# Optimization experiments

Hardware: AMD Instinct MI355X
Metric: run time of the kernel (lower is better)

The kernel has to match this reference:

```python
import math
import jax, jax.numpy as jnp
import numpy as np
from jax import lax

B, IMG, CIN, ED, TD, M = 32, 224, 3, 64, 64, 32
DILATIONS = (1, 2, 3, 4)
KS, STRIDE = 7, 4


def _conv2d(x, w, b, stride, pad, dil=1):
    y = lax.conv_general_dilated(x, w, (stride, stride), [(pad, pad), (pad, pad)],
                                 rhs_dilation=(dil, dil),
                                 dimension_numbers=('NCHW', 'OIHW', 'NCHW'))
    return y + b[None, :, None, None]


def _ln(x, g, b):
    mu = x.mean(-1, keepdims=True)
    var = ((x - mu) ** 2).mean(-1, keepdims=True)
    return (x - mu) / jnp.sqrt(var + 1e-5) * g + b


def setup_inputs() -> dict:
    key = jax.random.key(0)
    ks = jax.random.split(key, 25)
    s = 0.05
    rn = lambda k, shp: (jax.random.normal(k, shp) * s).astype(jnp.float32)
    inp = {}
    inp['x'] = jax.random.normal(ks[0], (B, CIN, IMG, IMG), dtype=jnp.float32)
    # PRM dilated conv weights (stacked over 4 dilations)
    inp['prm_w'] = rn(ks[1], (4, ED, CIN, KS, KS))
    inp['prm_b'] = rn(ks[2], (4, ED))
    # PCM stem: conv-SiLU, conv-BN-SiLU, conv-SiLU
    inp['pcm_w1'] = rn(ks[3], (ED, CIN, 3, 3))
    inp['pcm_b1'] = rn(ks[4], (ED,))
    inp['pcm_w2'] = rn(ks[5], (ED, ED, 3, 3))
    inp['pcm_b2'] = rn(ks[6], (ED,))
    inp['bn_g'] = 1.0 + rn(ks[7], (ED,))
    inp['bn_b'] = rn(ks[8], (ED,))
    inp['bn_mean'] = rn(ks[9], (ED,))
    inp['bn_var'] = jax.random.uniform(ks[10], (ED,), minval=0.5, maxval=1.5).astype(jnp.float32)
    inp['pcm_w3'] = rn(ks[11], (TD, ED, 3, 3))
    inp['pcm_b3'] = rn(ks[12], (TD,))
    # Token_performer params (dim = 4*ED = 256, emb = TD = 64, m = 32)
    dim = 4 * ED
    inp['ln1_g'] = 1.0 + rn(ks[13], (dim,))
    inp['ln1_b'] = rn(ks[14], (dim,))
    inp['kqv_w'] = rn(ks[15], (3 * TD, dim))
    inp['kqv_b'] = rn(ks[16], (3 * TD,))
    # orthogonal random-feature matrix, rows orthonormal, scaled by sqrt(m)
    a = np.random.default_rng(0).normal(size=(TD, TD))
    qmat, _ = np.linalg.qr(a)
    inp['w_perf'] = jnp.asarray(qmat[:M] * math.sqrt(M), dtype=jnp.float32)
    inp['proj_w'] = rn(ks[17], (TD, TD))
    inp['proj_b'] = rn(ks[18], (TD,))
    inp['ln2_g'] = 1.0 + rn(ks[19], (TD,))
    inp['ln2_b'] = rn(ks[20], (TD,))
    inp['mlp_w1'] = rn(ks[21], (TD, TD))
    inp['mlp_b1'] = rn(ks[22], (TD,))
    inp['mlp_w2'] = rn(ks[23], (TD, TD))
    inp['mlp_b2'] = rn(ks[24], (TD,))
    inp['H'] = IMG
    inp['W'] = IMG
    return inp


def reference(x, prm_w, prm_b, pcm_w1, pcm_b1, pcm_w2, pcm_b2, bn_g, bn_b, bn_mean,
              bn_var, pcm_w3, pcm_b3, ln1_g, ln1_b, kqv_w, kqv_b, w_perf, proj_w,
              proj_b, ln2_g, ln2_b, mlp_w1, mlp_b1, mlp_w2, mlp_b2, H, W):
    Bx = x.shape[0]
    Hp, Wp = H // STRIDE, W // STRIDE
    # --- PRM: parallel dilated Conv2d + GELU branches ---
    branches = []
    for i, d in enumerate(DILATIONS):  # fixed small set of structurally distinct convs
        pad = math.ceil(((KS - 1) * d + 1 - STRIDE) / 2)
        branches.append(jax.nn.gelu(_conv2d(x, prm_w[i], prm_b[i], STRIDE, pad, d),
                                    approximate=False))
    y = jnp.stack(branches, axis=1)  # [B, 4, ED, Hp, Wp]
    prm_x = y.reshape(Bx, len(DILATIONS) * ED, Hp * Wp).transpose(0, 2, 1)  # [B, N, 256]
    # --- PCM stem: conv-SiLU / conv-BN-SiLU / conv-SiLU (eval-mode BN) ---
    c = jax.nn.silu(_conv2d(x, pcm_w1, pcm_b1, 2, 1))
    c = _conv2d(c, pcm_w2, pcm_b2, 2, 1)
    inv = (bn_g / jnp.sqrt(bn_var + 1e-5))[None, :, None, None]
    c = (c - bn_mean[None, :, None, None]) * inv + bn_b[None, :, None, None]
    c = jax.nn.silu(c)
    c = jax.nn.silu(_conv2d(c, pcm_w3, pcm_b3, 1, 1))  # [B, TD, Hp, Wp]
    convX = c.transpose(0, 2, 3, 1).reshape(Bx, Hp * Wp, TD)
    # --- Performer kernelized attention ---
    xn = _ln(prm_x, ln1_g, ln1_b)
    kqv = xn @ kqv_w.T + kqv_b
    k, q, v = kqv[..., :TD], kqv[..., TD:2 * TD], kqv[..., 2 * TD:]

    def prm_exp(z):
        xd = 0.5 * (z * z).sum(-1, keepdims=True)          # [B, N, 1]
        wtx = jnp.einsum('bti,mi->btm', z, w_perf)          # [B, N, M]
        return jnp.exp(wtx - xd) / math.sqrt(M)

    kp, qp = prm_exp(k), prm_exp(q)                         # [B, N, M]
    D = jnp.einsum('btm,bm->bt', qp, kp.sum(axis=1))[..., None]  # [B, N, 1]
    kptv = jnp.einsum('btn,btm->bnm', v, kp)                # [B, TD, M]
    ya = jnp.einsum('btm,bnm->btn', qp, kptv) / (D + 1e-8)  # [B, N, TD]
    ya = v + ya @ proj_w.T + proj_b
    # --- combine + MLP block ---
    xo = ya + convX
    h = _ln(xo, ln2_g, ln2_b)
    h = jax.nn.gelu(h @ mlp_w1.T + mlp_b1, approximate=False) @ mlp_w2.T + mlp_b2
    return xo + h
```

## Files before the change

### kernel.cpp

```cpp
#include <hip/hip_runtime.h>
#include <hip/hip_bf16.h>
#include <cstddef>

#define BB    32
#define IMG   224
#define CIN   3
#define ED    64
#define TD    64
#define MM    32
#define HP    56
#define TT    3136
#define C4    256
#define KQVN  192

typedef __attribute__((ext_vector_type(8))) short bf16x8;
typedef __attribute__((ext_vector_type(4))) float f32x4;

#define OFF_CONVX  0u
#define OFF_XN     6422528u
#define OFF_C2B    6422528u
#define OFF_C1B    19267584u
#define OFF_V      19267584u
#define OFF_KP     25690112u
#define OFF_QP     28901376u
#define OFF_PART   32112640u
#define OFF_KPTV   33161216u
#define OFF_KPSP   (OFF_KPTV + 32768u)
#define OFF_WPJB   (OFF_KPTV + 49152u)
#define OFF_WM1B   (OFF_KPTV + 51200u)
#define OFF_WM2B   (OFF_KPTV + 53248u)
#define OFF_KPSUM  33226752u
#define OFF_WPT    (OFF_PART)
#define OFF_WKB    (OFF_PART + 37632u)
#define OFF_WC2B   (OFF_PART + 62208u)
#define OFF_WT3B   (OFF_PART + 80640u)
#define OFF_WC1B   (OFF_PART + 99072u)

__device__ __forceinline__ float geluf(float v){
  return 0.5f*v*(1.f + erff(v*0.70710678118654752f));
}
__device__ __forceinline__ float siluf(float v){
  return v/(1.f + expf(-v));
}
__device__ __forceinline__ ushort bfbits(float v){
  __hip_bfloat16 h = __float2bfloat16(v);
  return *reinterpret_cast<ushort*>(&h);
}

__global__ __launch_bounds__(256) void k_wtrans(
    const float* __restrict__ prm_w, const float* __restrict__ kqv_w,
    const float* __restrict__ pcm_w2, const float* __restrict__ pcm_w3,
    const float* __restrict__ pcm_w1, const float* __restrict__ proj_w,
    const float* __restrict__ mlp_w1, const float* __restrict__ mlp_w2,
    float* __restrict__ wpt, __hip_bfloat16* __restrict__ wkb,
    __hip_bfloat16* __restrict__ wc2b, __hip_bfloat16* __restrict__ wt3b,
    __hip_bfloat16* __restrict__ wc1b, __hip_bfloat16* __restrict__ wpjb,
    __hip_bfloat16* __restrict__ wm1b, __hip_bfloat16* __restrict__ wm2b)
{
  int idx = blockIdx.x*256 + threadIdx.x;
  if (idx < 37632){
    int oc = idx & 63, r = idx >> 6;
    int i = r/147, tap = r - i*147;
    wpt[idx] = prm_w[(i*64 + oc)*147 + tap];
  } else if (idx < 86784){
    int i4 = idx - 37632;
    wkb[i4] = __float2bfloat16(kqv_w[i4]);
  } else if (idx < 123648){
    int i2 = idx - 86784;
    int oc = i2/576, rem = i2 - oc*576;
    int khkw = rem >> 6, ci = rem & 63;
    int kh = khkw/3, kw = khkw - kh*3;
    wc2b[i2] = __float2bfloat16(pcm_w2[(oc*64+ci)*9 + kh*3 + kw]);
  } else if (idx < 160512){
    int i3 = idx - 123648;
    int oc = i3/576, rem = i3 - oc*576;
    int khkw = rem >> 6, ci = rem & 63;
    int kh = khkw/3, kw = khkw - kh*3;
    wt3b[i3] = __float2bfloat16(pcm_w3[(oc*64+ci)*9 + kh*3 + kw]);
  } else if (idx < 162560){
    int i5 = idx - 160512;
    int oc = i5 >> 5, k = i5 & 31;
    float v = 0.f;
    if (k < 27) v = pcm_w1[oc*27 + k];
    wc1b[i5] = __float2bfloat16(v);
  } else if (idx < 166656){
    wpjb[idx - 162560] = __float2bfloat16(proj_w[idx - 162560]);
  } else if (idx < 170752){
    wm1b[idx - 166656] = __float2bfloat16(mlp_w1[idx - 166656]);
  } else if (idx < 174848){
    wm2b[idx - 170752] = __float2bfloat16(mlp_w2[idx - 170752]);
  }
}

__global__ __launch_bounds__(256) void k_conv1(
    const float* __restrict__ x, const __hip_bfloat16* __restrict__ wc1b,
    const float* __restrict__ bias, __hip_bfloat16* __restrict__ c1b)
{
  __shared__ __align__(16) ushort xs[3*17*18];
  __shared__ __align__(16) ushort As[64*40];
  const int t = threadIdx.x;
  const int b = blockIdx.y;
  const int th = blockIdx.x/14, tw = blockIdx.x - th*14;
  const int oh0 = th*8, ow0 = tw*8;
  const int ih0 = oh0*2 - 1, iw0 = ow0*2 - 1;
  const int w = t>>6, lane = t&63, l15 = lane&15, hi = lane>>4;

  const float* xb = x + (size_t)b*CIN*IMG*IMG;
  for (int idx = t; idx < 918; idx += 256){
    int ci = idx/306, rem = idx - ci*306;
    int r = rem/18, c = rem - r*18;
    float v = 0.f;
    int ih = ih0 + r, iw = iw0 + c;
    if (c < 17 && (unsigned)ih < 224u && (unsigned)iw < 224u)
      v = xb[(ci*IMG+ih)*IMG+iw];
    xs[idx] = bfbits(v);
  }
  __syncthreads();
  for (int idx = t; idx < 2048; idx += 256){
    int pos = idx >> 5, k = idx & 31;
    ushort v = 0;
    if (k < 27){
      int ci = k/9, rem = k - ci*9;
      int kh = rem/3, kw = rem - kh*3;
      v = xs[(ci*17 + (pos>>3)*2 + kh)*18 + (pos&7)*2 + kw];
    }
    As[pos*40 + k] = v;
  }
  __syncthreads();

  float bs4[4];
  #pragma unroll
  for (int nb=0;nb<4;++nb) bs4[nb] = bias[nb*16+l15];
  f32x4 acc[4];
  #pragma unroll
  for (int nb=0;nb<4;++nb) acc[nb] = (f32x4){0.f,0.f,0.f,0.f};
  const ushort* wq = (const ushort*)wc1b;
  {
    bf16x8 a = *(const bf16x8*)&As[(w*16+l15)*40 + hi*8];
    #pragma unroll
    for (int nb=0;nb<4;++nb){
      bf16x8 bv = *(const bf16x8*)&wq[(nb*16+l15)*32 + hi*8];
      acc[nb] = __builtin_amdgcn_mfma_f32_16x16x32_bf16(a, bv, acc[nb], 0, 0, 0);
    }
  }
  #pragma unroll
  for (int nb=0;nb<4;++nb){
    #pragma unroll
    for (int r=0;r<4;++r){
      int row = w*16 + hi*4 + r;
      int oh = oh0 + (row>>3), ow = ow0 + (row&7);
      c1b[(((size_t)b*112+oh)*112+ow)*64 + nb*16+l15] =
        __float2bfloat16(siluf(acc[nb][r] + bs4[nb]));
    }
  }
}

__global__ __launch_bounds__(256) void k_conv2(
    const __hip_bfloat16* __restrict__ c1b, const __hip_bfloat16* __restrict__ wc2b,
    const float* __restrict__ bias, const float* __restrict__ g,
    const float* __restrict__ bb, const float* __restrict__ mean,
    const float* __restrict__ var, __hip_bfloat16* __restrict__ c2b)
{
  __shared__ __align__(16) ushort xs[17*17*72];
  const int b = blockIdx.y;
  const int th = blockIdx.x/7, tw = blockIdx.x - th*7;
  const int oh0 = th*8, ow0 = tw*8;
  const int t = threadIdx.x;
  const int w = t>>6, lane = t&63, l15 = lane&15, hi = lane>>4;

  const int ih0 = oh0*2-1, iw0 = ow0*2-1;
  const ushort* c1u = (const ushort*)c1b;
  for (int seg = t; seg < 2312; seg += 256){
    int pos = seg >> 3, s8 = seg & 7;
    int r = pos/17, c = pos - r*17;
    int ih = ih0 + r, iw = iw0 + c;
    uint4 val = {0,0,0,0};
    if ((unsigned)ih < 112u && (unsigned)iw < 112u)
      val = *(const uint4*)&c1u[(((size_t)b*112+ih)*112+iw)*64 + s8*8];
    *(uint4*)&xs[(r*17+c)*72 + s8*8] = val;
  }
  __syncthreads();

  float bs4[4], iv4[4], mn4[4], bo4[4];
  #pragma unroll
  for (int nb=0;nb<4;++nb){
    int oc = nb*16+l15;
    bs4[nb] = bias[oc];
    iv4[nb] = g[oc]*rsqrtf(var[oc]+1e-5f);
    mn4[nb] = mean[oc];
    bo4[nb] = bb[oc];
  }

  f32x4 acc[4];
  #pragma unroll
  for (int nb=0;nb<4;++nb) acc[nb] = (f32x4){0.f,0.f,0.f,0.f};

  const int p = w*16 + l15, pr = p>>3, pc = p&7;
  const ushort* wq = (const ushort*)wc2b;

  for (int ks=0; ks<18; ++ks){
    const int k0 = ks*32 + hi*8;
    const int khkw = k0 >> 6, ci0 = k0 & 63;
    const int kh = khkw/3, kw = khkw - kh*3;
    bf16x8 a = *(const bf16x8*)&xs[((2*pr+kh)*17 + 2*pc+kw)*72 + ci0];
    #pragma unroll
    for (int nb=0;nb<4;++nb){
      bf16x8 bv = *(const bf16x8*)&wq[(nb*16+l15)*576 + k0];
      acc[nb] = __builtin_amdgcn_mfma_f32_16x16x32_bf16(a, bv, acc[nb], 0, 0, 0);
    }
  }

  #pragma unroll
  for (int nb=0;nb<4;++nb){
    #pragma unroll
    for (int r=0;r<4;++r){
      int pp = w*16 + hi*4 + r;
      int oh = oh0 + (pp>>3), ow = ow0 + (pp&7);
      float vv = acc[nb][r] + bs4[nb];
      vv = (vv - mn4[nb])*iv4[nb] + bo4[nb];
      c2b[(((size_t)b*56+oh)*56+ow)*64 + nb*16+l15] = __float2bfloat16(siluf(vv));
    }
  }
}

__global__ __launch_bounds__(256) void k_conv3(
    const __hip_bfloat16* __restrict__ c2b, const __hip_bfloat16* __restrict__ wt3b,
    const float* __restrict__ bias, float* __restrict__ convX)
{
  __shared__ __align__(16) ushort xs[10*12*72];
  const int b = blockIdx.y;
  const int th = blockIdx.x/7, tw = blockIdx.x - th*7;
  const int oh0 = th*8, ow0 = tw*8;
  const int t = threadIdx.x;
  const int w = t>>6, lane = t&63, l15 = lane&15, hi = lane>>4;

  const ushort* c2u = (const ushort*)c2b;
  for (int seg = t; seg < 960; seg += 256){
    int pos = seg >> 3, s8 = seg & 7;
    int r = pos/12, c = pos - r*12;
    int ih = oh0 - 1 + r, iw = ow0 - 1 + c;
    uint4 val = {0,0,0,0};
    if ((unsigned)ih < 56u && (unsigned)iw < 56u)
      val = *(const uint4*)&c2u[(((size_t)b*56+ih)*56+iw)*64 + s8*8];
    *(uint4*)&xs[(r*12+c)*72 + s8*8] = val;
  }
  __syncthreads();

  float bs4[4];
  #pragma unroll
  for (int nb=0;nb<4;++nb) bs4[nb] = bias[nb*16+l15];

  f32x4 acc[4];
  #pragma unroll
  for (int nb=0;nb<4;++nb) acc[nb] = (f32x4){0.f,0.f,0.f,0.f};

  const int p = w*16 + l15, pr = p>>3, pc = p&7;
  const ushort* wq = (const ushort*)wt3b;

  for (int ks=0; ks<18; ++ks){
    const int k0 = ks*32 + hi*8;
    const int khkw = k0 >> 6, ci0 = k0 & 63;
    const int kh = khkw/3, kw = khkw - kh*3;
    bf16x8 a = *(const bf16x8*)&xs[((pr+kh)*12 + pc+kw)*72 + ci0];
    #pragma unroll
    for (int nb=0;nb<4;++nb){
      bf16x8 bv = *(const bf16x8*)&wq[(nb*16+l15)*576 + k0];
      acc[nb] = __builtin_amdgcn_mfma_f32_16x16x32_bf16(a, bv, acc[nb], 0, 0, 0);
    }
  }

  #pragma unroll
  for (int nb=0;nb<4;++nb){
    #pragma unroll
    for (int r=0;r<4;++r){
      int pp = w*16 + hi*4 + r;
      int oh = oh0 + (pp>>3), ow = ow0 + (pp&7);
      int s = oh*HP + ow;
      convX[((size_t)b*TT + s)*64 + nb*16+l15] = siluf(acc[nb][r] + bs4[nb]);
    }
  }
}

#define LOADX(PH) do{ const float4* xr_ = (const float4*)(rowb + (PH)*20); \
  *(float4*)&X[0]=xr_[0]; *(float4*)&X[4]=xr_[1]; *(float4*)&X[8]=xr_[2]; \
  *(float4*)&X[12]=xr_[3]; *(float4*)&X[16]=xr_[4]; }while(0)
#define TAP(KW,Q0) do{ const float wv_ = wrow[(KW)*64]; \
  v[0]+=wv_*X[(Q0)+0];  v[1]+=wv_*X[(Q0)+1];  v[2]+=wv_*X[(Q0)+2];  v[3]+=wv_*X[(Q0)+3]; \
  v[4]+=wv_*X[(Q0)+4];  v[5]+=wv_*X[(Q0)+5];  v[6]+=wv_*X[(Q0)+6];  v[7]+=wv_*X[(Q0)+7]; \
  v[8]+=wv_*X[(Q0)+8];  v[9]+=wv_*X[(Q0)+9];  v[10]+=wv_*X[(Q0)+10]; v[11]+=wv_*X[(Q0)+11]; \
  v[12]+=wv_*X[(Q0)+12]; v[13]+=wv_*X[(Q0)+13]; }while(0)

template<int D>
__device__ __forceinline__ void prm_core(const float* __restrict__ xt2,
    const float* __restrict__ wq, float v[14])
{
  constexpr int R0 = 12 - 3*D;
  #pragma unroll 1
  for (int ci=0; ci<3; ++ci){
    #pragma unroll 1
    for (int kh=0; kh<7; ++kh){
      const float* rowb = xt2 + ci*2000 + (R0 + kh*D)*80;
      const float* wrow = wq + ((ci*7+kh)*7)*64;
      float X[20];
      if constexpr (D == 1){
        LOADX(0); TAP(3,3);
        LOADX(1); TAP(0,2); TAP(4,3);
        LOADX(2); TAP(1,2); TAP(5,3);
        LOADX(3); TAP(2,2); TAP(6,3);
      } else if constexpr (D == 2){
        LOADX(0); TAP(1,2); TAP(3,3); TAP(5,4);
        LOADX(2); TAP(0,1); TAP(2,2); TAP(4,3); TAP(6,4);
      } else if constexpr (D == 3){
        LOADX(0); TAP(3,3);
        LOADX(1); TAP(2,2); TAP(6,5);
        LOADX(2); TAP(1,1); TAP(5,4);
        LOADX(3); TAP(0,0); TAP(4,3);
      } else {
        LOADX(0); TAP(0,0); TAP(1,1); TAP(2,2); TAP(3,3); TAP(4,4); TAP(5,5); TAP(6,6);
      }
    }
  }
}

__global__ __launch_bounds__(256) void k_prm_ln(
    const float* __restrict__ x, const float* __restrict__ wpt,
    const float* __restrict__ prm_b, const float* __restrict__ ln_g,
    const float* __restrict__ ln_b, __hip_bfloat16* __restrict__ xn)
{
  __shared__ __align__(16) float xt2[6000];
  __shared__ float wred[4][14][2];
  const int t = threadIdx.x;
  const int b = blockIdx.y;
  const int oh  = blockIdx.x >> 2;
  const int owt = blockIdx.x & 3;
  const int ow0 = owt*14;
  const int ih0 = oh*4 - 11;
  const int iw0 = ow0*4 - 11;

  const float* xb = x + (size_t)b*CIN*IMG*IMG;
  for (int idx = t; idx < 6000; idx += 256){
    int ci  = idx / 2000;
    int rem = idx - ci*2000;
    int r   = rem / 80;
    int cc  = rem - r*80;
    int ih = ih0 + r, iw = iw0 + cc;
    float val = 0.f;
    if ((unsigned)ih < (unsigned)IMG && (unsigned)iw < (unsigned)IMG)
      val = xb[(ci*IMG+ih)*IMG+iw];
    xt2[(ci*25 + r)*80 + (cc&3)*20 + (cc>>2)] = val;
  }
  __syncthreads();

  const int i = t >> 6, lane = t & 63;
  float v[14];
  const float bi = prm_b[i*64+lane];
  #pragma unroll
  for (int p=0;p<14;++p) v[p] = bi;
  const float* wq = wpt + (i*147)*64 + lane;

  if      (i == 0) prm_core<1>(xt2, wq, v);
  else if (i == 1) prm_core<2>(xt2, wq, v);
  else if (i == 2) prm_core<3>(xt2, wq, v);
  else             prm_core<4>(xt2, wq, v);

  #pragma unroll
  for (int p=0;p<14;++p) v[p] = geluf(v[p]);
  #pragma unroll
  for (int p=0;p<14;++p){
    float s1 = v[p], s2 = v[p]*v[p];
    #pragma unroll
    for (int o=32;o;o>>=1){
      s1 += __shfl_xor(s1, o, 64);
      s2 += __shfl_xor(s2, o, 64);
    }
    if (lane == 0){ wred[i][p][0] = s1; wred[i][p][1] = s2; }
  }
  __syncthreads();
  const float lg = ln_g[t], lb = ln_b[t];
  const int s_base = oh*HP + ow0;
  #pragma unroll
  for (int p=0;p<14;++p){
    float S1 = wred[0][p][0]+wred[1][p][0]+wred[2][p][0]+wred[3][p][0];
    float S2 = wred[0][p][1]+wred[1][p][1]+wred[2][p][1]+wred[3][p][1];
    float mu = S1*(1.f/256.f);
    float rs = rsqrtf(S2*(1.f/256.f) - mu*mu + 1e-5f);
    float outv = (v[p]-mu)*rs*lg + lb;
    xn[((size_t)(b*TT + s_base + p))*256 + t] = __float2bfloat16(outv);
  }
}

__global__ __launch_bounds__(256) void k_kqv_perf(
    const __hip_bfloat16* __restrict__ xn, const __hip_bfloat16* __restrict__ wkb,
    const float* __restrict__ kqv_b, const float* __restrict__ wperf,
    float* __restrict__ v_g, float* __restrict__ kp, float* __restrict__ qp)
{
  __shared__ __align__(16) char smem[36864];
  __shared__ float wperf_s[32*68];
  __shared__ float kqvb_s[192];
  __shared__ float xd_s[128];
  ushort* As = (ushort*)smem;
  ushort* Bs = (ushort*)(smem + 9216);
  float*  zq = (float*)smem;

  const int t = threadIdx.x;
  const int m0 = blockIdx.x*64;
  const int w = t >> 6, lane = t & 63;
  const int l15 = lane & 15, hi = lane >> 4;

  for (int idx = t; idx < 2048; idx += 256)
    wperf_s[(idx>>6)*68 + (idx&63)] = wperf[idx];
  if (t < 192) kqvb_s[t] = kqv_b[t];

  f32x4 acc[12];
  #pragma unroll
  for (int nb=0;nb<12;++nb) acc[nb] = (f32x4){0.f,0.f,0.f,0.f};

  const ushort* xnu = (const ushort*)xn;
  const ushort* wku = (const ushort*)wkb;

  for (int kc=0; kc<4; ++kc){
    #pragma unroll
    for (int ss=0; ss<2; ++ss){
      int seg = ss*256 + t;
      int row = seg >> 3, c8 = seg & 7;
      *(uint4*)&As[row*72 + c8*8] =
        *(const uint4*)&xnu[((size_t)(m0+row))*256 + kc*64 + c8*8];
    }
    #pragma unroll
    for (int ss=0; ss<6; ++ss){
      int seg = ss*256 + t;
      int row = seg >> 3, c8 = seg & 7;
      *(uint4*)&Bs[row*72 + c8*8] =
        *(const uint4*)&wku[row*256 + kc*64 + c8*8];
    }
    __syncthreads();
    #pragma unroll
    for (int ks=0; ks<2; ++ks){
      bf16x8 a = *(const bf16x8*)&As[(16*w + l15)*72 + ks*32 + hi*8];
      #pragma unroll
      for (int nb=0;nb<12;++nb){
        bf16x8 bv = *(const bf16x8*)&Bs[(nb*16 + l15)*72 + ks*32 + hi*8];
        acc[nb] = __builtin_amdgcn_mfma_f32_16x16x32_bf16(a, bv, acc[nb], 0, 0, 0);
      }
    }
    __syncthreads();
  }

  #pragma unroll
  for (int nb=0;nb<12;++nb){
    int col = nb*16 + l15;
    float bias = kqvb_s[col];
    #pragma unroll
    for (int r=0;r<4;++r){
      int row = w*16 + hi*4 + r;
      float val = acc[nb][r] + bias;
      if (col < 128) zq[row*132 + col] = val;
      else v_g[((size_t)(m0+row))*64 + (col-128)] = val;
    }
  }
  __syncthreads();

  if (t < 128){
    int pos = t & 63, wh = t >> 6;
    const float4* zr4 = (const float4*)&zq[pos*132 + wh*64];
    float s = 0.f;
    #pragma unroll
    for (int c4=0;c4<16;++c4){
      float4 z4 = zr4[c4];
      s += z4.x*z4.x + z4.y*z4.y + z4.z*z4.z + z4.w*z4.w;
    }
    xd_s[t] = 0.5f*s;
  }
  __syncthreads();

  {
    const int qi = t >> 1, mbase = (t & 1)*16;
    const int pos = qi & 63, wh = qi >> 6;
    const float4* zr4 = (const float4*)&zq[pos*132 + wh*64];
    float wtx[16];
    #pragma unroll
    for (int j=0;j<16;++j) wtx[j] = 0.f;
    #pragma unroll 4
    for (int c4=0;c4<16;++c4){
      float4 z4 = zr4[c4];
      #pragma unroll
      for (int j=0;j<16;++j){
        const float4 w4 = *(const float4*)&wperf_s[(mbase+j)*68 + c4*4];
        wtx[j] += z4.x*w4.x + z4.y*w4.y + z4.z*w4.z + z4.w*w4.w;
      }
    }
    const float xd = xd_s[qi];
    float* dst = wh ? qp : kp;
    float* dp = dst + ((size_t)(m0+pos))*32 + mbase;
    #pragma unroll
    for (int j4=0;j4<4;++j4){
      float4 o;
      o.x = expf(wtx[j4*4+0] - xd) * 0.17677669529663687f;
      o.y = expf(wtx[j4*4+1] - xd) * 0.17677669529663687f;
      o.z = expf(wtx[j4*4+2] - xd) * 0.17677669529663687f;
      o.w = expf(wtx[j4*4+3] - xd) * 0.17677669529663687f;
      *(float4*)&dp[j4*4] = o;
    }
  }
}

__global__ __launch_bounds__(256) void k_kptv(
    const float* __restrict__ v_g, const float* __restrict__ kp,
    float* __restrict__ part, float* __restrict__ kpsum_part)
{
  __shared__ __align__(16) ushort vT[64*232];
  __shared__ __align__(16) ushort kpT[32*232];
  __shared__ float ksh[8][32];
  const int b = blockIdx.y, g = blockIdx.x;
  const int t = threadIdx.x;
  const int w = t>>6, lane = t&63, l15 = lane&15, hi = lane>>4;
  const int t0 = g*196;

  for (int idx = t; idx < 14336; idx += 256){
    int tt = idx >> 6, n = idx & 63;
    float vv = (tt < 196) ? v_g[((size_t)b*TT + t0 + tt)*64 + n] : 0.f;
    vT[n*232 + tt] = bfbits(vv);
  }
  for (int idx = t; idx < 7168; idx += 256){
    int tt = idx >> 5, m = idx & 31;
    float kv = (tt < 196) ? kp[((size_t)b*TT + t0 + tt)*32 + m] : 0.f;
    kpT[m*232 + tt] = bfbits(kv);
  }
  __syncthreads();

  f32x4 accp[2];
  accp[0] = (f32x4){0.f,0.f,0.f,0.f};
  accp[1] = (f32x4){0.f,0.f,0.f,0.f};
  for (int ks=0; ks<7; ++ks){
    bf16x8 a = *(const bf16x8*)&vT[(w*16+l15)*232 + ks*32 + hi*8];
    #pragma unroll
    for (int nt=0; nt<2; ++nt){
      bf16x8 bv = *(const bf16x8*)&kpT[(nt*16+l15)*232 + ks*32 + hi*8];
      accp[nt] = __builtin_amdgcn_mfma_f32_16x16x32_bf16(a, bv, accp[nt], 0, 0, 0);
    }
  }
  #pragma unroll
  for (int nt=0;nt<2;++nt){
    #pragma unroll
    for (int r=0;r<4;++r){
      int row = w*16 + hi*4 + r;
      int col = nt*16 + l15;
      part[(((size_t)g*BB + b)*64 + row)*MM + col] = accp[nt][r];
    }
  }
  {
    int m = t & 31, h8 = t >> 5;
    float s = 0.f;
    int lo = h8*25, hic = lo+25 < 196 ? lo+25 : 196;
    for (int tt = lo; tt < hic; ++tt){
      ushort u = kpT[m*232 + tt];
      __hip_bfloat16 hv = *reinterpret_cast<__hip_bfloat16*>(&u);
      s += __bfloat162float(hv);
    }
    ksh[h8][m] = s;
  }
  __syncthreads();
  if (t < 32){
    float s = 0.f;
    #pragma unroll
    for (int j=0;j<8;++j) s += ksh[j][t];
    kpsum_part[(size_t)g*1024 + b*32 + t] = s;
  }
}

__global__ __launch_bounds__(256) void k_kptv_red(
    const float* __restrict__ part, const float* __restrict__ kpsum_part,
    __hip_bfloat16* __restrict__ kptvb, float* __restrict__ kpsum)
{
  const int t = threadIdx.x;
  const int idx = blockIdx.x*256 + t;
  float a = 0.f;
  #pragma unroll
  for (int g=0; g<16; ++g) a += part[(size_t)g*65536 + idx];
  kptvb[idx] = __float2bfloat16(a);
  if (blockIdx.x < 4){
    int kidx = blockIdx.x*256 + t;
    float s = 0.f;
    #pragma unroll
    for (int g=0; g<16; ++g) s += kpsum_part[(size_t)g*1024 + kidx];
    kpsum[kidx] = s;
  }
}

__global__ __launch_bounds__(256) void k_attn_mlp(
    const float* __restrict__ v_g, const float* __restrict__ qp,
    const float* __restrict__ kpsum, const __hip_bfloat16* __restrict__ kptvb,
    const __hip_bfloat16* __restrict__ wpjb, const float* __restrict__ projb,
    const float* __restrict__ convX,
    const float* __restrict__ ln2_g, const float* __restrict__ ln2_b,
    const __hip_bfloat16* __restrict__ wm1b, const float* __restrict__ b1,
    const __hip_bfloat16* __restrict__ wm2b, const float* __restrict__ b2,
    float* __restrict__ out)
{
  __shared__ __align__(16) char smem[64512];
  ushort* qpb = (ushort*)smem;
  ushort* ktb = (ushort*)(smem + 5120);
  ushort* pjw = (ushort*)(smem + 10240);
  ushort* hb  = (ushort*)smem;
  ushort* t2  = (ushort*)(smem + 19456);
  ushort* w1b = (ushort*)(smem + 28672);
  ushort* w2b = (ushort*)(smem + 37888);
  float*  xosh= (float*)(smem + 47104);
  __shared__ float Ds[64];
  __shared__ float Dp[4][64];
  __shared__ float ks_s[32], pjb_s[64], b1_s[64], b2_s[64], g2_s[64], bb2_s[64];

  const int t = threadIdx.x;
  const int b = blockIdx.y;
  const int p0 = blockIdx.x*64;
  const int w = t>>6, lane = t&63, l15 = lane&15, hi = lane>>4;

  const float* qpg = qp + ((size_t)b*TT + p0)*32;
  for (int idx = t; idx < 2048; idx += 256)
    qpb[(idx>>5)*40 + (idx&31)] = bfbits(qpg[idx]);
  const ushort* ktg = (const ushort*)kptvb + (size_t)b*2048;
  for (int idx = t; idx < 2048; idx += 256)
    ktb[(idx>>5)*40 + (idx&31)] = ktg[idx];
  const ushort* pju = (const ushort*)wpjb;
  const ushort* w1u = (const ushort*)wm1b;
  const ushort* w2u = (const ushort*)wm2b;
  for (int idx = t; idx < 4096; idx += 256){
    pjw[(idx>>6)*72 + (idx&63)] = pju[idx];
    w1b[(idx>>6)*72 + (idx&63)] = w1u[idx];
    w2b[(idx>>6)*72 + (idx&63)] = w2u[idx];
  }
  if (t < 32) ks_s[t] = kpsum[b*MM + t];
  if (t < 64){
    pjb_s[t] = projb[t]; b1_s[t] = b1[t]; b2_s[t] = b2[t];
    g2_s[t] = ln2_g[t];  bb2_s[t] = ln2_b[t];
  }
  __syncthreads();

  {
    int pos = t & 63, grp = t >> 6;
    float s = 0.f;
    #pragma unroll
    for (int j=0;j<8;++j){
      int m = grp*8 + j;
      __hip_bfloat16 h = *reinterpret_cast<__hip_bfloat16*>(&qpb[pos*40 + m]);
      s += __bfloat162float(h) * ks_s[m];
    }
    Dp[grp][pos] = s;
  }
  __syncthreads();
  if (t < 64) Ds[t] = Dp[0][t]+Dp[1][t]+Dp[2][t]+Dp[3][t] + 1e-8f;
  __syncthreads();

  f32x4 acc1[4];
  #pragma unroll
  for (int nb=0;nb<4;++nb) acc1[nb] = (f32x4){0.f,0.f,0.f,0.f};
  {
    bf16x8 a = *(const bf16x8*)&qpb[(w*16 + l15)*40 + hi*8];
    #pragma unroll
    for (int nb=0;nb<4;++nb){
      bf16x8 bv = *(const bf16x8*)&ktb[(nb*16 + l15)*40 + hi*8];
      acc1[nb] = __builtin_amdgcn_mfma_f32_16x16x32_bf16(a, bv, acc1[nb], 0, 0, 0);
    }
  }
  #pragma unroll
  for (int nb=0;nb<4;++nb){
    #pragma unroll
    for (int r=0;r<4;++r){
      int row = w*16 + hi*4 + r;
      t2[row*72 + nb*16 + l15] = bfbits(acc1[nb][r] / Ds[row]);
    }
  }
  __syncthreads();

  f32x4 acc2[4];
  #pragma unroll
  for (int nb=0;nb<4;++nb) acc2[nb] = (f32x4){0.f,0.f,0.f,0.f};
  #pragma unroll
  for (int ks=0; ks<2; ++ks){
    bf16x8 a2 = *(const bf16x8*)&t2[(w*16 + l15)*72 + ks*32 + hi*8];
    #pragma unroll
    for (int nb=0;nb<4;++nb){
      bf16x8 bv2 = *(const bf16x8*)&pjw[(nb*16 + l15)*72 + ks*32 + hi*8];
      acc2[nb] = __builtin_amdgcn_mfma_f32_16x16x32_bf16(a2, bv2, acc2[nb], 0, 0, 0);
    }
  }
  #pragma unroll
  for (int nb=0;nb<4;++nb){
    #pragma unroll
    for (int r=0;r<4;++r){
      int row = w*16 + hi*4 + r;
      int col = nb*16 + l15;
      const size_t off = ((size_t)b*TT + p0 + row)*64 + col;
      xosh[row*68 + col] = v_g[off] + acc2[nb][r] + pjb_s[col] + convX[off];
    }
  }
  __syncthreads();

  {
    const int n = t & 63, p = t >> 6;
    const float g2 = g2_s[n], bb2 = bb2_s[n];
    for (int sp=0; sp<16; ++sp){
      const int pos = sp*4 + p;
      const float xv = xosh[pos*68 + n];
      float s1 = xv, s2 = xv*xv;
      #pragma unroll
      for (int o=32;o;o>>=1){
        s1 += __shfl_xor(s1, o, 64);
        s2 += __shfl_xor(s2, o, 64);
      }
      float mu = s1*(1.f/64.f);
      float rs = rsqrtf(s2*(1.f/64.f) - mu*mu + 1e-5f);
      t2[pos*72 + n] = bfbits((xv - mu)*rs*g2 + bb2);
    }
  }
  __syncthreads();

  f32x4 acc3[4];
  #pragma unroll
  for (int nb=0;nb<4;++nb) acc3[nb] = (f32x4){0.f,0.f,0.f,0.f};
  #pragma unroll
  for (int ks=0; ks<2; ++ks){
    bf16x8 a3 = *(const bf16x8*)&t2[(w*16 + l15)*72 + ks*32 + hi*8];
    #pragma unroll
    for (int nb=0;nb<4;++nb){
      bf16x8 bv3 = *(const bf16x8*)&w1b[(nb*16 + l15)*72 + ks*32 + hi*8];
      acc3[nb] = __builtin_amdgcn_mfma_f32_16x16x32_bf16(a3, bv3, acc3[nb], 0, 0, 0);
    }
  }
  __syncthreads();
  #pragma unroll
  for (int nb=0;nb<4;++nb){
    #pragma unroll
    for (int r=0;r<4;++r){
      int row = w*16 + hi*4 + r;
      int col = nb*16 + l15;
      hb[row*72 + col] = bfbits(geluf(acc3[nb][r] + b1_s[col]));
    }
  }
  __syncthreads();

  f32x4 acc4[4];
  #pragma unroll
  for (int nb=0;nb<4;++nb) acc4[nb] = (f32x4){0.f,0.f,0.f,0.f};
  #pragma unroll
  for (int ks=0; ks<2; ++ks){
    bf16x8 a4 = *(const bf16x8*)&hb[(w*16 + l15)*72 + ks*32 + hi*8];
    #pragma unroll
    for (int nb=0;nb<4;++nb){
      bf16x8 bv4 = *(const bf16x8*)&w2b[(nb*16 + l15)*72 + ks*32 + hi*8];
      acc4[nb] = __builtin_amdgcn_mfma_f32_16x16x32_bf16(a4, bv4, acc4[nb], 0, 0, 0);
    }
  }
  #pragma unroll
  for (int nb=0;nb<4;++nb){
    #pragma unroll
    for (int r=0;r<4;++r){
      int row = w*16 + hi*4 + r;
      int col = nb*16 + l15;
      const size_t off = ((size_t)b*TT + p0 + row)*64 + col;
      out[off] = xosh[row*68 + col] + acc4[nb][r] + b2_s[col];
    }
  }
}

extern "C" void kernel_launch(void* const* d_in, const int* in_sizes, int n_in,
                              void* d_out, int out_size, void* d_ws, size_t ws_size,
                              hipStream_t stream)
{
  const float* x      = (const float*)d_in[0];
  const float* prm_w  = (const float*)d_in[1];
  const float* prm_b  = (const float*)d_in[2];
  const float* pcm_w1 = (const float*)d_in[3];
  const float* pcm_b1 = (const float*)d_in[4];
  const float* pcm_w2 = (const float*)d_in[5];
  const float* pcm_b2 = (const float*)d_in[6];
  const float* bn_g   = (const float*)d_in[7];
  const float* bn_b   = (const float*)d_in[8];
  const float* bn_mean= (const float*)d_in[9];
  const float* bn_var = (const float*)d_in[10];
  const float* pcm_w3 = (const float*)d_in[11];
  const float* pcm_b3 = (const float*)d_in[12];
  const float* ln1_g  = (const float*)d_in[13];
  const float* ln1_b  = (const float*)d_in[14];
  const float* kqv_w  = (const float*)d_in[15];
  const float* kqv_b  = (const float*)d_in[16];
  const float* w_perf = (const float*)d_in[17];
  const float* proj_w = (const float*)d_in[18];
  const float* proj_b = (const float*)d_in[19];
  const float* ln2_g  = (const float*)d_in[20];
  const float* ln2_b  = (const float*)d_in[21];
  const float* mlp_w1 = (const float*)d_in[22];
  const float* mlp_b1 = (const float*)d_in[23];
  const float* mlp_w2 = (const float*)d_in[24];
  const float* mlp_b2 = (const float*)d_in[25];

  float* ws = (float*)d_ws;
  float* convX = ws + OFF_CONVX;
  __hip_bfloat16* xn  = (__hip_bfloat16*)(ws + OFF_XN);
  __hip_bfloat16* c2b = (__hip_bfloat16*)(ws + OFF_C2B);
  __hip_bfloat16* c1b = (__hip_bfloat16*)(ws + OFF_C1B);
  float* v_g   = ws + OFF_V;
  float* kp    = ws + OFF_KP;
  float* qp    = ws + OFF_QP;
  float* part  = ws + OFF_PART;
  __hip_bfloat16* kptvb = (__hip_bfloat16*)(ws + OFF_KPTV);
  float* kpsum_part = ws + OFF_KPSP;
  float* kpsum = ws + OFF_KPSUM;
  float* wpt   = ws + OFF_WPT;
  __hip_bfloat16* wkb  = (__hip_bfloat16*)(ws + OFF_WKB);
  __hip_bfloat16* wc2b = (__hip_bfloat16*)(ws + OFF_WC2B);
  __hip_bfloat16* wt3b = (__hip_bfloat16*)(ws + OFF_WT3B);
  __hip_bfloat16* wc1b = (__hip_bfloat16*)(ws + OFF_WC1B);
  __hip_bfloat16* wpjb = (__hip_bfloat16*)(ws + OFF_WPJB);
  __hip_bfloat16* wm1b = (__hip_bfloat16*)(ws + OFF_WM1B);
  __hip_bfloat16* wm2b = (__hip_bfloat16*)(ws + OFF_WM2B);
  float* out   = (float*)d_out;

  k_wtrans<<<dim3(683), 256, 0, stream>>>(prm_w, kqv_w, pcm_w2, pcm_w3, pcm_w1,
                                          proj_w, mlp_w1, mlp_w2,
                                          wpt, wkb, wc2b, wt3b, wc1b,
                                          wpjb, wm1b, wm2b);
  k_conv1<<<dim3(196,BB), 256, 0, stream>>>(x, wc1b, pcm_b1, c1b);
  k_conv2<<<dim3(49,BB), 256, 0, stream>>>(c1b, wc2b, pcm_b2, bn_g, bn_b,
                                           bn_mean, bn_var, c2b);
  k_conv3<<<dim3(49,BB), 256, 0, stream>>>(c2b, wt3b, pcm_b3, convX);
  k_prm_ln<<<dim3(224,BB), 256, 0, stream>>>(x, wpt, prm_b, ln1_g, ln1_b, xn);
  k_kqv_perf<<<dim3(1568), 256, 0, stream>>>(xn, wkb, kqv_b, w_perf, v_g, kp, qp);
  k_kptv<<<dim3(16,BB), 256, 0, stream>>>(v_g, kp, part, kpsum_part);
  k_kptv_red<<<dim3(256), 256, 0, stream>>>(part, kpsum_part, kptvb, kpsum);
  k_attn_mlp<<<dim3(49,BB), 256, 0, stream>>>(v_g, qp, kpsum, kptvb, wpjb, proj_b,
                                              convX, ln2_g, ln2_b, wm1b, mlp_b1,
                                              wm2b, mlp_b2, out);
}
```

Before: 494.8 us.

## Use split-bf16 MFMA for performer projection, store convX as bf16, split PRM launch

The performer random-feature projection moves from scalar fp32 FMA loops to MFMA. Both z and w_perf are split into bf16 high and low parts, and three MFMAs per tile keep roughly fp32 accuracy. convX is now written and read as bf16, which halves its memory traffic, at some cost in precision on the residual path. The PRM+LN kernel is also launched as two half-batch grids, and a few bf16-to-float conversions use a cheaper bit shift.

```diff
diff --git a/kernel.cpp b/kernel.cpp
--- a/kernel.cpp
+++ b/kernel.cpp
@@ -29,6 +29,8 @@
 #define OFF_WPJB   (OFF_KPTV + 49152u)
 #define OFF_WM1B   (OFF_KPTV + 51200u)
 #define OFF_WM2B   (OFF_KPTV + 53248u)
+#define OFF_WPFH   (OFF_KPTV + 55296u)
+#define OFF_WPFL   (OFF_KPTV + 56320u)
 #define OFF_KPSUM  33226752u
 #define OFF_WPT    (OFF_PART)
 #define OFF_WKB    (OFF_PART + 37632u)
@@ -46,16 +48,21 @@
   __hip_bfloat16 h = __float2bfloat16(v);
   return *reinterpret_cast<ushort*>(&h);
 }
+__device__ __forceinline__ float bf2f(ushort u){
+  return __uint_as_float(((unsigned)u) << 16);
+}
 
 __global__ __launch_bounds__(256) void k_wtrans(
     const float* __restrict__ prm_w, const float* __restrict__ kqv_w,
     const float* __restrict__ pcm_w2, const float* __restrict__ pcm_w3,
     const float* __restrict__ pcm_w1, const float* __restrict__ proj_w,
     const float* __restrict__ mlp_w1, const float* __restrict__ mlp_w2,
+    const float* __restrict__ wperf,
     float* __restrict__ wpt, __hip_bfloat16* __restrict__ wkb,
     __hip_bfloat16* __restrict__ wc2b, __hip_bfloat16* __restrict__ wt3b,
     __hip_bfloat16* __restrict__ wc1b, __hip_bfloat16* __restrict__ wpjb,
-    __hip_bfloat16* __restrict__ wm1b, __hip_bfloat16* __restrict__ wm2b)
+    __hip_bfloat16* __restrict__ wm1b, __hip_bfloat16* __restrict__ wm2b,
+    __hip_bfloat16* __restrict__ wpfh, __hip_bfloat16* __restrict__ wpfl)
 {
   int idx = blockIdx.x*256 + threadIdx.x;
   if (idx < 37632){
@@ -89,6 +96,14 @@
     wm1b[idx - 166656] = __float2bfloat16(mlp_w1[idx - 166656]);
   } else if (idx < 174848){
     wm2b[idx - 170752] = __float2bfloat16(mlp_w2[idx - 170752]);
+  } else if (idx < 176896){
+    int i6 = idx - 174848;
+    wpfh[i6] = __float2bfloat16(wperf[i6]);
+  } else if (idx < 178944){
+    int i7 = idx - 176896;
+    float v = wperf[i7];
+    float h = bf2f(bfbits(v));
+    wpfl[i7] = __float2bfloat16(v - h);
   }
 }
 
@@ -225,7 +240,7 @@
 
 __global__ __launch_bounds__(256) void k_conv3(
     const __hip_bfloat16* __restrict__ c2b, const __hip_bfloat16* __restrict__ wt3b,
-    const float* __restrict__ bias, float* __restrict__ convX)
+    const float* __restrict__ bias, __hip_bfloat16* __restrict__ convXb)
 {
   __shared__ __align__(16) ushort xs[10*12*72];
   const int b = blockIdx.y;
@@ -276,7 +291,8 @@
       int pp = w*16 + hi*4 + r;
       int oh = oh0 + (pp>>3), ow = ow0 + (pp&7);
       int s = oh*HP + ow;
-      convX[((size_t)b*TT + s)*64 + nb*16+l15] = siluf(acc[nb][r] + bs4[nb]);
+      convXb[((size_t)b*TT + s)*64 + nb*16+l15] =
+        __float2bfloat16(siluf(acc[nb][r] + bs4[nb]));
     }
   }
 }
@@ -325,12 +341,12 @@
 __global__ __launch_bounds__(256) void k_prm_ln(
     const float* __restrict__ x, const float* __restrict__ wpt,
     const float* __restrict__ prm_b, const float* __restrict__ ln_g,
-    const float* __restrict__ ln_b, __hip_bfloat16* __restrict__ xn)
+    const float* __restrict__ ln_b, __hip_bfloat16* __restrict__ xn, int b0)
 {
   __shared__ __align__(16) float xt2[6000];
   __shared__ float wred[4][14][2];
   const int t = threadIdx.x;
-  const int b = blockIdx.y;
+  const int b = blockIdx.y + b0;
   const int oh  = blockIdx.x >> 2;
   const int owt = blockIdx.x & 3;
   const int ow0 = owt*14;
@@ -391,24 +407,32 @@
 
 __global__ __launch_bounds__(256) void k_kqv_perf(
     const __hip_bfloat16* __restrict__ xn, const __hip_bfloat16* __restrict__ wkb,
-    const float* __restrict__ kqv_b, const float* __restrict__ wperf,
+    const float* __restrict__ kqv_b,
+    const __hip_bfloat16* __restrict__ wpfh, const __hip_bfloat16* __restrict__ wpfl,
     float* __restrict__ v_g, float* __restrict__ kp, float* __restrict__ qp)
 {
   __shared__ __align__(16) char smem[36864];
-  __shared__ float wperf_s[32*68];
+  __shared__ __align__(16) ushort wph[32*72];
+  __shared__ __align__(16) ushort wpl[32*72];
   __shared__ float kqvb_s[192];
   __shared__ float xd_s[128];
-  ushort* As = (ushort*)smem;
-  ushort* Bs = (ushort*)(smem + 9216);
-  float*  zq = (float*)smem;
+  ushort* As  = (ushort*)smem;
+  ushort* Bs  = (ushort*)(smem + 9216);
+  ushort* zhb = (ushort*)smem;
+  ushort* zlb = (ushort*)(smem + 18432);
 
   const int t = threadIdx.x;
   const int m0 = blockIdx.x*64;
   const int w = t >> 6, lane = t & 63;
   const int l15 = lane & 15, hi = lane >> 4;
 
-  for (int idx = t; idx < 2048; idx += 256)
-    wperf_s[(idx>>6)*68 + (idx&63)] = wperf[idx];
+  const ushort* wph_g = (const ushort*)wpfh;
+  const ushort* wpl_g = (const ushort*)wpfl;
+  for (int idx = t; idx < 2048; idx += 256){
+    int row = idx >> 6, c = idx & 63;
+    wph[row*72 + c] = wph_g[idx];
+    wpl[row*72 + c] = wpl_g[idx];
+  }
   if (t < 192) kqvb_s[t] = kqv_b[t];
 
   f32x4 acc[12];
@@ -454,52 +478,71 @@
     for (int r=0;r<4;++r){
       int row = w*16 + hi*4 + r;
       float val = acc[nb][r] + bias;
-      if (col < 128) zq[row*132 + col] = val;
-      else v_g[((size_t)(m0+row))*64 + (col-128)] = val;
+      if (col < 128){
+        int zrow = (col >> 6)*64 + row;
+        int zc = col & 63;
+        ushort zh = bfbits(val);
+        zhb[zrow*72 + zc] = zh;
+        zlb[zrow*72 + zc] = bfbits(val - bf2f(zh));
+      } else {
+        v_g[((size_t)(m0+row))*64 + (col-128)] = val;
+      }
     }
   }
   __syncthreads();
 
   if (t < 128){
-    int pos = t & 63, wh = t >> 6;
-    const float4* zr4 = (const float4*)&zq[pos*132 + wh*64];
     float s = 0.f;
     #pragma unroll
-    for (int c4=0;c4<16;++c4){
-      float4 z4 = zr4[c4];
-      s += z4.x*z4.x + z4.y*z4.y + z4.z*z4.z + z4.w*z4.w;
+    for (int c8=0;c8<8;++c8){
+      bf16x8 zh8 = *(const bf16x8*)&zhb[t*72 + c8*8];
+      bf16x8 zl8 = *(const bf16x8*)&zlb[t*72 + c8*8];
+      #pragma unroll
+      for (int j=0;j<8;++j){
+        float z = bf2f((ushort)zh8[j]) + bf2f((ushort)zl8[j]);
+        s += z*z;
+      }
     }
     xd_s[t] = 0.5f*s;
   }
   __syncthreads();
 
-  {
-    const int qi = t >> 1, mbase = (t & 1)*16;
-    const int pos = qi & 63, wh = qi >> 6;
-    const float4* zr4 = (const float4*)&zq[pos*132 + wh*64];
-    float wtx[16];
-    #pragma unroll
-    for (int j=0;j<16;++j) wtx[j] = 0.f;
-    #pragma unroll 4
-    for (int c4=0;c4<16;++c4){
-      float4 z4 = zr4[c4];
+  f32x4 accd[2][2];
+  #pragma unroll
+  for (int ri=0;ri<2;++ri)
+    #pragma unroll
+    for (int nb=0;nb<2;++nb) accd[ri][nb] = (f32x4){0.f,0.f,0.f,0.f};
+  #pragma unroll
+  for (int ri=0;ri<2;++ri){
+    const int rb = 2*w + ri;
+    #pragma unroll
+    for (int ks=0;ks<2;++ks){
+      bf16x8 ah = *(const bf16x8*)&zhb[(rb*16 + l15)*72 + ks*32 + hi*8];
+      bf16x8 al = *(const bf16x8*)&zlb[(rb*16 + l15)*72 + ks*32 + hi*8];
       #pragma unroll
-      for (int j=0;j<16;++j){
-        const float4 w4 = *(const float4*)&wperf_s[(mbase+j)*68 + c4*4];
-        wtx[j] += z4.x*w4.x + z4.y*w4.y + z4.z*w4.z + z4.w*w4.w;
+      for (int nb=0;nb<2;++nb){
+        bf16x8 bh = *(const bf16x8*)&wph[(nb*16 + l15)*72 + ks*32 + hi*8];
+        bf16x8 bl = *(const bf16x8*)&wpl[(nb*16 + l15)*72 + ks*32 + hi*8];
+        accd[ri][nb] = __builtin_amdgcn_mfma_f32_16x16x32_bf16(ah, bh, accd[ri][nb], 0, 0, 0);
+        accd[ri][nb] = __builtin_amdgcn_mfma_f32_16x16x32_bf16(al, bh, accd[ri][nb], 0, 0, 0);
+        accd[ri][nb] = __builtin_amdgcn_mfma_f32_16x16x32_bf16(ah, bl, accd[ri][nb], 0, 0, 0);
       }
     }
-    const float xd = xd_s[qi];
-    float* dst = wh ? qp : kp;
-    float* dp = dst + ((size_t)(m0+pos))*32 + mbase;
-    #pragma unroll
-    for (int j4=0;j4<4;++j4){
-      float4 o;
-      o.x = expf(wtx[j4*4+0] - xd) * 0.17677669529663687f;
-      o.y = expf(wtx[j4*4+1] - xd) * 0.17677669529663687f;
-      o.z = expf(wtx[j4*4+2] - xd) * 0.17677669529663687f;
-      o.w = expf(wtx[j4*4+3] - xd) * 0.17677669529663687f;
-      *(float4*)&dp[j4*4] = o;
+  }
+  #pragma unroll
+  for (int ri=0;ri<2;++ri){
+    const int rb = 2*w + ri;
+    #pragma unroll
+    for (int nb=0;nb<2;++nb){
+      const int m = nb*16 + l15;
+      #pragma unroll
+      for (int r=0;r<4;++r){
+        int row = rb*16 + hi*4 + r;
+        int wh = row >> 6, pos = row & 63;
+        float outv = expf(accd[ri][nb][r] - xd_s[row]) * 0.17677669529663687f;
+        float* dst = wh ? qp : kp;
+        dst[((size_t)(m0+pos))*32 + m] = outv;
+      }
     }
   }
 }
@@ -553,9 +596,7 @@
     float s = 0.f;
     int lo = h8*25, hic = lo+25 < 196 ? lo+25 : 196;
     for (int tt = lo; tt < hic; ++tt){
-      ushort u = kpT[m*232 + tt];
-      __hip_bfloat16 hv = *reinterpret_cast<__hip_bfloat16*>(&u);
-      s += __bfloat162float(hv);
+      s += bf2f(kpT[m*232 + tt]);
     }
     ksh[h8][m] = s;
   }
@@ -591,7 +632,7 @@
     const float* __restrict__ v_g, const float* __restrict__ qp,
     const float* __restrict__ kpsum, const __hip_bfloat16* __restrict__ kptvb,
     const __hip_bfloat16* __restrict__ wpjb, const float* __restrict__ projb,
-    const float* __restrict__ convX,
+    const __hip_bfloat16* __restrict__ convXb,
     const float* __restrict__ ln2_g, const float* __restrict__ ln2_b,
     const __hip_bfloat16* __restrict__ wm1b, const float* __restrict__ b1,
     const __hip_bfloat16* __restrict__ wm2b, const float* __restrict__ b2,
@@ -642,8 +683,7 @@
     #pragma unroll
     for (int j=0;j<8;++j){
       int m = grp*8 + j;
-      __hip_bfloat16 h = *reinterpret_cast<__hip_bfloat16*>(&qpb[pos*40 + m]);
-      s += __bfloat162float(h) * ks_s[m];
+      s += bf2f(qpb[pos*40 + m]) * ks_s[m];
     }
     Dp[grp][pos] = s;
   }
@@ -684,6 +724,7 @@
       acc2[nb] = __builtin_amdgcn_mfma_f32_16x16x32_bf16(a2, bv2, acc2[nb], 0, 0, 0);
     }
   }
+  const ushort* cxu = (const ushort*)convXb;
   #pragma unroll
   for (int nb=0;nb<4;++nb){
     #pragma unroll
@@ -691,7 +732,7 @@
       int row = w*16 + hi*4 + r;
       int col = nb*16 + l15;
       const size_t off = ((size_t)b*TT + p0 + row)*64 + col;
-      xosh[row*68 + col] = v_g[off] + acc2[nb][r] + pjb_s[col] + convX[off];
+      xosh[row*68 + col] = v_g[off] + acc2[nb][r] + pjb_s[col] + bf2f(cxu[off]);
     }
   }
   __syncthreads();
@@ -795,7 +836,7 @@
   const float* mlp_b2 = (const float*)d_in[25];
 
   float* ws = (float*)d_ws;
-  float* convX = ws + OFF_CONVX;
+  __hip_bfloat16* convXb = (__hip_bfloat16*)(ws + OFF_CONVX);
   __hip_bfloat16* xn  = (__hip_bfloat16*)(ws + OFF_XN);
   __hip_bfloat16* c2b = (__hip_bfloat16*)(ws + OFF_C2B);
   __hip_bfloat16* c1b = (__hip_bfloat16*)(ws + OFF_C1B);
@@ -814,21 +855,24 @@
   __hip_bfloat16* wpjb = (__hip_bfloat16*)(ws + OFF_WPJB);
   __hip_bfloat16* wm1b = (__hip_bfloat16*)(ws + OFF_WM1B);
   __hip_bfloat16* wm2b = (__hip_bfloat16*)(ws + OFF_WM2B);
+  __hip_bfloat16* wpfh = (__hip_bfloat16*)(ws + OFF_WPFH);
+  __hip_bfloat16* wpfl = (__hip_bfloat16*)(ws + OFF_WPFL);
   float* out   = (float*)d_out;
 
-  k_wtrans<<<dim3(683), 256, 0, stream>>>(prm_w, kqv_w, pcm_w2, pcm_w3, pcm_w1,
-                                          proj_w, mlp_w1, mlp_w2,
+  k_wtrans<<<dim3(699), 256, 0, stream>>>(prm_w, kqv_w, pcm_w2, pcm_w3, pcm_w1,
+                                          proj_w, mlp_w1, mlp_w2, w_perf,
                                           wpt, wkb, wc2b, wt3b, wc1b,
-                                          wpjb, wm1b, wm2b);
+                                          wpjb, wm1b, wm2b, wpfh, wpfl);
   k_conv1<<<dim3(196,BB), 256, 0, stream>>>(x, wc1b, pcm_b1, c1b);
   k_conv2<<<dim3(49,BB), 256, 0, stream>>>(c1b, wc2b, pcm_b2, bn_g, bn_b,
                                            bn_mean, bn_var, c2b);
-  k_conv3<<<dim3(49,BB), 256, 0, stream>>>(c2b, wt3b, pcm_b3, convX);
-  k_prm_ln<<<dim3(224,BB), 256, 0, stream>>>(x, wpt, prm_b, ln1_g, ln1_b, xn);
-  k_kqv_perf<<<dim3(1568), 256, 0, stream>>>(xn, wkb, kqv_b, w_perf, v_g, kp, qp);
+  k_conv3<<<dim3(49,BB), 256, 0, stream>>>(c2b, wt3b, pcm_b3, convXb);
+  k_prm_ln<<<dim3(224,16), 256, 0, stream>>>(x, wpt, prm_b, ln1_g, ln1_b, xn, 0);
+  k_prm_ln<<<dim3(224,16), 256, 0, stream>>>(x, wpt, prm_b, ln1_g, ln1_b, xn, 16);
+  k_kqv_perf<<<dim3(1568), 256, 0, stream>>>(xn, wkb, kqv_b, wpfh, wpfl, v_g, kp, qp);
   k_kptv<<<dim3(16,BB), 256, 0, stream>>>(v_g, kp, part, kpsum_part);
   k_kptv_red<<<dim3(256), 256, 0, stream>>>(part, kpsum_part, kptvb, kpsum);
   k_attn_mlp<<<dim3(49,BB), 256, 0, stream>>>(v_g, qp, kpsum, kptvb, wpjb, proj_b,
-                                              convX, ln2_g, ln2_b, wm1b, mlp_b1,
+                                              convXb, ln2_g, ln2_b, wm1b, mlp_b1,
                                               wm2b, mlp_b2, out);
 }
```

After: 484.9 us. 2.0% less time.
